# Performance work log

Hardware: AMD Instinct MI355X
Metric: run time of the kernel (lower is better)

Reference implementation:

```python
import jax, jax.numpy as jnp
from jax import lax
import numpy as np

C = 56; DI = 112; DS = 16; R = 4; K = 4; NB = 10; UP = 3
B, H, W = 1, 64, 64

def conv2d(x, w, b=None, pad=1, groups=1):
    out = lax.conv_general_dilated(x, w, (1, 1), [(pad, pad), (pad, pad)],
                                   feature_group_count=groups,
                                   dimension_numbers=('NCHW', 'OIHW', 'NCHW'))
    if b is not None:
        out = out + b[None, :, None, None]
    return out

def ln_last(x, w, b, eps=1e-5):
    mu = x.mean(-1, keepdims=True)
    var = ((x - mu) ** 2).mean(-1, keepdims=True)
    return (x - mu) / jnp.sqrt(var + eps) * w + b

def ln_cf(x, w, b, eps=1e-6):
    mu = x.mean(1, keepdims=True)
    var = ((x - mu) ** 2).mean(1, keepdims=True)
    return (x - mu) / jnp.sqrt(var + eps) * w[None, :, None, None] + b[None, :, None, None]

def bsconv(x, pw_w, dw_w, dw_b):
    x = conv2d(x, pw_w, pad=0)
    return conv2d(x, dw_w, dw_b, pad=1, groups=dw_w.shape[0])

def ss2d(x, p):
    # x: (B,H,W,C) -> SS2D (VMamba 4-direction selective scan)
    b, h, w, _ = x.shape
    L = h * w
    xz = x @ p['inproj_w'].T                        # (B,H,W,2*DI)
    xin, z = jnp.split(xz, 2, axis=-1)
    xc = jnp.transpose(xin, (0, 3, 1, 2))           # (B,DI,H,W)
    xc = jax.nn.silu(conv2d(xc, p['conv_w'], p['conv_b'], pad=1, groups=DI))
    xf = xc.reshape(b, DI, L)
    xt = jnp.swapaxes(xc, 2, 3).reshape(b, DI, L)
    x_hwwh = jnp.stack([xf, xt], axis=1)            # (B,2,DI,L)
    xs = jnp.concatenate([x_hwwh, jnp.flip(x_hwwh, -1)], axis=1)  # (B,K,DI,L)
    x_dbl = jnp.einsum('bkdl,kcd->bkcl', xs, p['xproj_w'])
    dts, Bs, Cs = jnp.split(x_dbl, [R, R + DS], axis=2)
    dts = jnp.einsum('bkrl,kdr->bkdl', dts, p['dt_w'])
    A = -jnp.exp(p['Alog'].reshape(K, DI, DS))
    delta = jax.nn.softplus(dts + p['dt_b'][None, :, :, None])    # (B,K,DI,L)

    def step(hst, inp):
        dl, xl, bl, cl = inp
        dA = jnp.exp(dl[..., None] * A[None])       # (B,K,DI,DS)
        hst = dA * hst + (dl * xl)[..., None] * bl[:, :, None, :]
        y = jnp.einsum('bkdn,bkn->bkd', hst, cl)
        return hst, y

    seq = (jnp.transpose(delta, (3, 0, 1, 2)), jnp.transpose(xs, (3, 0, 1, 2)),
           jnp.transpose(Bs, (3, 0, 1, 2)), jnp.transpose(Cs, (3, 0, 1, 2)))
    h0 = jnp.zeros((b, K, DI, DS), x.dtype)
    _, ys = lax.scan(step, h0, seq)                 # (L,B,K,DI)
    out_y = jnp.transpose(ys, (1, 2, 3, 0)) + p['D'].reshape(K, DI)[None, :, :, None] * xs
    inv = jnp.flip(out_y[:, 2:4], -1)
    y1 = out_y[:, 0]
    y2 = inv[:, 0]
    y3 = jnp.swapaxes(inv[:, 1].reshape(b, DI, w, h), 2, 3).reshape(b, DI, L)
    y4 = jnp.swapaxes(out_y[:, 1].reshape(b, DI, w, h), 2, 3).reshape(b, DI, L)
    y = jnp.swapaxes(y1 + y2 + y3 + y4, 1, 2).reshape(b, h, w, DI)
    y = ln_last(y, p['onorm_w'], p['onorm_b'])
    y = y * jax.nn.silu(z)
    return y @ p['outproj_w'].T

def safm(x, mfr_w, mfr_b, aggr_w, aggr_b):
    b, c, h, w = x.shape
    ch = c // 4
    parts = jnp.split(x, 4, axis=1)
    outs = []
    for i in range(4):
        s = parts[i]
        f = 2 ** i
        if i > 0:
            s = s.reshape(b, ch, h // f, f, w // f, f).max(axis=(3, 5))
        s = conv2d(s, mfr_w[i], mfr_b[i], pad=1, groups=ch)
        if i > 0:
            s = jnp.repeat(jnp.repeat(s, f, axis=2), f, axis=3)
        outs.append(s)
    out = conv2d(jnp.concatenate(outs, axis=1), aggr_w, aggr_b, pad=0)
    return jax.nn.gelu(out, approximate=False) * x

def afd(x, p):
    xn = jnp.transpose(x, (0, 2, 3, 1))
    xn = xn + ss2d(ln_last(xn, p['ln1_w'], p['ln1_b']), p)   # VSSBlock residual
    x = jnp.transpose(xn, (0, 3, 1, 2))
    x = x + safm(ln_cf(x, p['norm_w'], p['norm_b']), p['mfr_w'], p['mfr_b'], p['aggr_w'], p['aggr_b'])
    return x, x

def _forward(x, fea_pw_w, fea_dw_w, fea_dw_b,
             blk_ln1_w, blk_ln1_b, blk_inproj_w, blk_conv_w, blk_conv_b,
             blk_xproj_w, blk_dt_w, blk_dt_b, blk_Alog, blk_D,
             blk_onorm_w, blk_onorm_b, blk_outproj_w,
             blk_norm_w, blk_norm_b, blk_mfr_w, blk_mfr_b, blk_aggr_w, blk_aggr_b,
             c1_w, c1_b, norm_w, norm_b, c2_pw_w, c2_dw_w, c2_dw_b, up_w, up_b):
    out_fea = bsconv(x, fea_pw_w, fea_dw_w, fea_dw_b)
    bp = {'ln1_w': blk_ln1_w, 'ln1_b': blk_ln1_b, 'inproj_w': blk_inproj_w,
          'conv_w': blk_conv_w, 'conv_b': blk_conv_b, 'xproj_w': blk_xproj_w,
          'dt_w': blk_dt_w, 'dt_b': blk_dt_b, 'Alog': blk_Alog, 'D': blk_D,
          'onorm_w': blk_onorm_w, 'onorm_b': blk_onorm_b, 'outproj_w': blk_outproj_w,
          'norm_w': blk_norm_w, 'norm_b': blk_norm_b, 'mfr_w': blk_mfr_w,
          'mfr_b': blk_mfr_b, 'aggr_w': blk_aggr_w, 'aggr_b': blk_aggr_b}
    _, outs = lax.scan(afd, out_fea, bp)            # (NB,B,C,H,W) in B1..B10 order
    b, _, h, w = out_fea.shape
    trunk = jnp.transpose(outs, (1, 0, 2, 3, 4)).reshape(b, NB * C, h, w)
    out_B = conv2d(trunk, c1_w, c1_b, pad=0)
    out_B = jax.nn.gelu(ln_cf(out_B, norm_w, norm_b), approximate=False)
    out_lr = bsconv(out_B, c2_pw_w, c2_dw_w, c2_dw_b) + out_fea
    up = conv2d(out_lr, up_w, up_b, pad=1)          # (B, 3*UP*UP, H, W)
    oc = up.shape[1] // (UP * UP)
    ps = up.reshape(b, oc, UP, UP, h, w)
    return jnp.transpose(ps, (0, 1, 4, 2, 5, 3)).reshape(b, oc, h * UP, w * UP)

def setup_inputs():
    key = jax.random.key(0)
    ks = iter(jax.random.split(key, 40))
    rn = lambda shape, s=0.05: jax.random.normal(next(ks), shape, jnp.float32) * s
    ones = lambda shape: jnp.ones(shape, jnp.float32)
    zeros = lambda shape: jnp.zeros(shape, jnp.float32)
    return {
        'x': jax.random.normal(next(ks), (B, 3, H, W), jnp.float32),
        'fea_pw_w': rn((C, 3, 1, 1), 0.3),
        'fea_dw_w': rn((C, 1, 3, 3), 0.3),
        'fea_dw_b': zeros((C,)),
        'blk_ln1_w': ones((NB, C)), 'blk_ln1_b': zeros((NB, C)),
        'blk_inproj_w': rn((NB, 2 * DI, C)),
        'blk_conv_w': rn((NB, DI, 1, 3, 3), 0.2), 'blk_conv_b': zeros((NB, DI)),
        'blk_xproj_w': rn((NB, K, R + 2 * DS, DI)),
        'blk_dt_w': rn((NB, K, DI, R), 0.2),
        'blk_dt_b': jnp.full((NB, K, DI), -4.6, jnp.float32),
        'blk_Alog': jnp.broadcast_to(jnp.log(jnp.arange(1, DS + 1, dtype=jnp.float32)), (NB, K * DI, DS)) + jnp.zeros((NB, K * DI, DS), jnp.float32),
        'blk_D': ones((NB, K * DI)),
        'blk_onorm_w': ones((NB, DI)), 'blk_onorm_b': zeros((NB, DI)),
        'blk_outproj_w': rn((NB, C, DI)),
        'blk_norm_w': ones((NB, C)), 'blk_norm_b': zeros((NB, C)),
        'blk_mfr_w': rn((NB, 4, C // 4, 1, 3, 3), 0.2), 'blk_mfr_b': zeros((NB, 4, C // 4)),
        'blk_aggr_w': rn((NB, C, C, 1, 1)), 'blk_aggr_b': zeros((NB, C)),
        'c1_w': rn((C, NB * C, 1, 1)), 'c1_b': zeros((C,)),
        'norm_w': ones((C,)), 'norm_b': zeros((C,)),
        'c2_pw_w': rn((C, C, 1, 1)), 'c2_dw_w': rn((C, 1, 3, 3), 0.2), 'c2_dw_b': zeros((C,)),
        'up_w': rn((3 * UP * UP, C, 3, 3)), 'up_b': zeros((3 * UP * UP,)),
    }

def reference(x, fea_pw_w, fea_dw_w, fea_dw_b,
              blk_ln1_w, blk_ln1_b, blk_inproj_w, blk_conv_w, blk_conv_b,
              blk_xproj_w, blk_dt_w, blk_dt_b, blk_Alog, blk_D,
              blk_onorm_w, blk_onorm_b, blk_outproj_w,
              blk_norm_w, blk_norm_b, blk_mfr_w, blk_mfr_b, blk_aggr_w, blk_aggr_b,
              c1_w, c1_b, norm_w, norm_b, c2_pw_w, c2_dw_w, c2_dw_b, up_w, up_b):
    return _forward(x, fea_pw_w, fea_dw_w, fea_dw_b,
                    blk_ln1_w, blk_ln1_b, blk_inproj_w, blk_conv_w, blk_conv_b,
                    blk_xproj_w, blk_dt_w, blk_dt_b, blk_Alog, blk_D,
                    blk_onorm_w, blk_onorm_b, blk_outproj_w,
                    blk_norm_w, blk_norm_b, blk_mfr_w, blk_mfr_b, blk_aggr_w, blk_aggr_b,
                    c1_w, c1_b, norm_w, norm_b, c2_pw_w, c2_dw_w, c2_dw_b, up_w, up_b)
```

## Files before the change

### kernel.cpp

```cpp
#include <hip/hip_runtime.h>
#include <hip/hip_bf16.h>

#define HW 64
#define L4 4096
#define CC 56
#define DI 112
#define DSN 16
#define NBLK 10

typedef const float* BP;

__device__ __forceinline__ float bf(BP p, int i) { return p[i]; }
__device__ __forceinline__ float siluf(float x) { return x / (1.f + __expf(-x)); }
__device__ __forceinline__ float geluf(float x) { return 0.5f * x * (1.f + erff(x * 0.70710678f)); }

__global__ void k_fea_pw(BP x, BP w, float* __restrict__ t0) {
    int tid = blockIdx.x * blockDim.x + threadIdx.x;
    if (tid >= CC * L4) return;
    int c = tid >> 12, l = tid & 4095;
    float acc = 0.f;
    for (int i = 0; i < 3; ++i) acc += bf(x, i * L4 + l) * bf(w, c * 3 + i);
    t0[tid] = acc;
}

__global__ void __launch_bounds__(256) k_dw3x3t(
        const float* __restrict__ src, BP w, BP bvec, float* __restrict__ dst,
        int act, const float* __restrict__ addsrc) {
    int c = blockIdx.x >> 4;
    int tile = blockIdx.x & 15;
    int y0 = (tile >> 2) * 16, x0 = (tile & 3) * 16;
    __shared__ float sT[18 * 18];
    const float* sc = src + (size_t)c * L4;
    for (int idx = threadIdx.x; idx < 324; idx += 256) {
        int iy = idx / 18, ix = idx - iy * 18;
        int gy = y0 - 1 + iy, gx = x0 - 1 + ix;
        sT[idx] = (gy >= 0 && gy < 64 && gx >= 0 && gx < 64) ? sc[gy * 64 + gx] : 0.f;
    }
    __syncthreads();
    int py = threadIdx.x >> 4, px = threadIdx.x & 15;
    BP wr = w + c * 9;
    float acc = bvec ? bvec[c] : 0.f;
    #pragma unroll
    for (int ky = 0; ky < 3; ++ky)
        #pragma unroll
        for (int kx = 0; kx < 3; ++kx)
            acc += sT[(py + ky) * 18 + px + kx] * wr[ky * 3 + kx];
    if (act) acc = siluf(acc);
    int l = (y0 + py) * 64 + x0 + px;
    if (addsrc) acc += addsrc[(size_t)c * L4 + l];
    dst[(size_t)c * L4 + l] = acc;
}

__global__ void __launch_bounds__(256) k_ln56g(
        const float* __restrict__ part, BP bias, BP w, BP b, float* __restrict__ dst) {
    int lane = threadIdx.x & 63;
    int cg = threadIdx.x >> 6;
    int l0 = blockIdx.x * 64;
    __shared__ float sS[56 * 64];
    __shared__ float sPa[4][64], sPb[4][64];
    __shared__ float sMu[64], sRs[64];
    float ps = 0.f, ps2 = 0.f;
    for (int c = cg * 14; c < cg * 14 + 14; ++c) {
        float v = bias[c];
        #pragma unroll
        for (int z = 0; z < 5; ++z)
            v += part[(size_t)(z * 56 + c) * L4 + l0 + lane];
        sS[c * 64 + lane] = v; ps += v; ps2 += v * v;
    }
    sPa[cg][lane] = ps; sPb[cg][lane] = ps2;
    __syncthreads();
    if (threadIdx.x < 64) {
        float s = sPa[0][lane] + sPa[1][lane] + sPa[2][lane] + sPa[3][lane];
        float s2 = sPb[0][lane] + sPb[1][lane] + sPb[2][lane] + sPb[3][lane];
        float mu = s / 56.f;
        float var = fmaxf(s2 / 56.f - mu * mu, 0.f);
        sMu[lane] = mu; sRs[lane] = rsqrtf(var + 1e-6f);
    }
    __syncthreads();
    float mu = sMu[lane], rs = sRs[lane];
    for (int c = cg * 14; c < cg * 14 + 14; ++c) {
        float v = (sS[c * 64 + lane] - mu) * rs * w[c] + b[c];
        dst[(size_t)c * L4 + l0 + lane] = geluf(v);
    }
}

__global__ void __launch_bounds__(256) k_gemm(
        const float* __restrict__ src, BP w, BP bvec, const float* __restrict__ addsrc,
        float* __restrict__ dst, int nin, int nout) {
    int lane = threadIdx.x & 63;
    int jg = threadIdx.x >> 6;
    int l0 = blockIdx.x * 64;
    int j0 = blockIdx.y * 16;
    __shared__ __align__(16) float sS[56 * 64];
    __shared__ __align__(16) float sw[16 * 56];
    float acc[4] = {0.f, 0.f, 0.f, 0.f};

    for (int i0 = 0; i0 < nin; i0 += 56) {
        __syncthreads();
        for (int idx = threadIdx.x; idx < 56 * 64; idx += 256) {
            int ii = idx >> 6, px = idx & 63;
            sS[idx] = src[(size_t)(i0 + ii) * L4 + l0 + px];
        }
        for (int idx = threadIdx.x; idx < 16 * 56; idx += 256) {
            int jj = idx / 56, ii = idx - jj * 56;
            int j = j0 + jj;
            sw[idx] = (j < nout) ? w[(size_t)j * nin + i0 + ii] : 0.f;
        }
        __syncthreads();
        #pragma unroll
        for (int ii = 0; ii < 56; ii += 4) {
            float s0 = sS[(ii + 0) * 64 + lane];
            float s1 = sS[(ii + 1) * 64 + lane];
            float s2 = sS[(ii + 2) * 64 + lane];
            float s3 = sS[(ii + 3) * 64 + lane];
            #pragma unroll
            for (int jj = 0; jj < 4; ++jj) {
                const float4 wv = *(const float4*)&sw[(jg * 4 + jj) * 56 + ii];
                acc[jj] += s0 * wv.x + s1 * wv.y + s2 * wv.z + s3 * wv.w;
            }
        }
    }
    int l = l0 + lane;
    #pragma unroll
    for (int jj = 0; jj < 4; ++jj) {
        int j = j0 + jg * 4 + jj;
        if (j >= nout) continue;
        float v = acc[jj];
        if (bvec) v += bf(bvec, j);
        size_t idx = (size_t)j * L4 + l;
        if (addsrc) v += addsrc[idx];
        dst[idx] = v;
    }
}

__global__ void __launch_bounds__(256) k_c1(
        const float* __restrict__ src, BP w, float* __restrict__ part) {
    int lane = threadIdx.x & 63;
    int jg = threadIdx.x >> 6;
    int l0 = blockIdx.x * 64;
    int j0 = blockIdx.y * 16;
    int z = blockIdx.z;
    __shared__ __align__(16) float sS[56 * 64];
    __shared__ __align__(16) float sw[16 * 56];
    float acc[4] = {0.f, 0.f, 0.f, 0.f};

    for (int i0 = z * 112; i0 < z * 112 + 112; i0 += 56) {
        __syncthreads();
        for (int idx = threadIdx.x; idx < 56 * 64; idx += 256) {
            int ii = idx >> 6, px = idx & 63;
            sS[idx] = src[(size_t)(i0 + ii) * L4 + l0 + px];
        }
        for (int idx = threadIdx.x; idx < 16 * 56; idx += 256) {
            int jj = idx / 56, ii = idx - jj * 56;
            int j = j0 + jj;
            sw[idx] = (j < 56) ? w[(size_t)j * 560 + i0 + ii] : 0.f;
        }
        __syncthreads();
        #pragma unroll
        for (int ii = 0; ii < 56; ii += 4) {
            float s0 = sS[(ii + 0) * 64 + lane];
            float s1 = sS[(ii + 1) * 64 + lane];
            float s2 = sS[(ii + 2) * 64 + lane];
            float s3 = sS[(ii + 3) * 64 + lane];
            #pragma unroll
            for (int jj = 0; jj < 4; ++jj) {
                const float4 wv = *(const float4*)&sw[(jg * 4 + jj) * 56 + ii];
                acc[jj] += s0 * wv.x + s1 * wv.y + s2 * wv.z + s3 * wv.w;
            }
        }
    }
    int l = l0 + lane;
    #pragma unroll
    for (int jj = 0; jj < 4; ++jj) {
        int j = j0 + jg * 4 + jj;
        if (j < 56) part[(size_t)(z * 56 + j) * L4 + l] = acc[jj];
    }
}

__global__ void __launch_bounds__(256) k_xproj(
        const float* __restrict__ src, BP w, float* __restrict__ dst) {
    int lane = threadIdx.x & 31;
    int jg = threadIdx.x >> 5;
    int l0 = blockIdx.x * 32;
    int j0 = blockIdx.y * 16;
    __shared__ __align__(16) float sS[112 * 32];
    __shared__ __align__(16) float sw[16 * 112];
    float acc[2] = {0.f, 0.f};

    for (int idx = threadIdx.x; idx < 112 * 32; idx += 256) {
        int ii = idx >> 5, px = idx & 31;
        sS[idx] = src[(size_t)ii * L4 + l0 + px];
    }
    for (int idx = threadIdx.x; idx < 16 * 112; idx += 256) {
        int jj = idx / 112, ii = idx - jj * 112;
        sw[idx] = w[(size_t)(j0 + jj) * 112 + ii];
    }
    __syncthreads();
    #pragma unroll
    for (int ii = 0; ii < 112; ii += 4) {
        float s0 = sS[(ii + 0) * 32 + lane];
        float s1 = sS[(ii + 1) * 32 + lane];
        float s2 = sS[(ii + 2) * 32 + lane];
        float s3 = sS[(ii + 3) * 32 + lane];
        #pragma unroll
        for (int jj = 0; jj < 2; ++jj) {
            const float4 wv = *(const float4*)&sw[(jg * 2 + jj) * 112 + ii];
            acc[jj] += s0 * wv.x + s1 * wv.y + s2 * wv.z + s3 * wv.w;
        }
    }
    __syncthreads();
    #pragma unroll
    for (int jj = 0; jj < 2; ++jj)
        sS[(jg * 2 + jj) * 32 + lane] = acc[jj];
    __syncthreads();
    for (int idx = threadIdx.x; idx < 16 * 32; idx += 256) {
        int cidx = idx & 15, l2 = idx >> 4;
        int j = j0 + cidx;
        int k = j / 36, c = j - k * 36;
        dst[((size_t)k * L4 + l0 + l2) * 36 + c] = sS[cidx * 32 + l2];
    }
}

__global__ void __launch_bounds__(256) k_gemm_ln(
        const float* __restrict__ src, BP lnw, BP lnb, BP w,
        float* __restrict__ dst, int nout) {
    int lane = threadIdx.x & 63;
    int jg = threadIdx.x >> 6;
    int l0 = blockIdx.x * 64;
    int j0 = blockIdx.y * 16;
    __shared__ __align__(16) float sS[56 * 64];
    __shared__ __align__(16) float sw[16 * 56];
    __shared__ float sLw[56], sLb[56];
    float acc[4] = {0.f, 0.f, 0.f, 0.f};

    for (int idx = threadIdx.x; idx < 56 * 64; idx += 256) {
        int ii = idx >> 6, px = idx & 63;
        sS[idx] = src[(size_t)ii * L4 + l0 + px];
    }
    for (int idx = threadIdx.x; idx < 16 * 56; idx += 256) {
        int jj = idx / 56, ii = idx - jj * 56;
        int j = j0 + jj;
        sw[idx] = (j < nout) ? w[(size_t)j * 56 + ii] : 0.f;
    }
    if (threadIdx.x < 56) { sLw[threadIdx.x] = lnw[threadIdx.x]; sLb[threadIdx.x] = lnb[threadIdx.x]; }
    __syncthreads();
    if (threadIdx.x < 64) {
        int px = threadIdx.x;
        float s = 0.f, s2 = 0.f;
        for (int ii = 0; ii < 56; ++ii) { float v = sS[ii * 64 + px]; s += v; s2 += v * v; }
        float mu = s / 56.f;
        float var = fmaxf(s2 / 56.f - mu * mu, 0.f);
        float rstd = rsqrtf(var + 1e-5f);
        for (int ii = 0; ii < 56; ++ii)
            sS[ii * 64 + px] = (sS[ii * 64 + px] - mu) * rstd * sLw[ii] + sLb[ii];
    }
    __syncthreads();
    #pragma unroll
    for (int ii = 0; ii < 56; ii += 4) {
        float s0 = sS[(ii + 0) * 64 + lane];
        float s1 = sS[(ii + 1) * 64 + lane];
        float s2 = sS[(ii + 2) * 64 + lane];
        float s3 = sS[(ii + 3) * 64 + lane];
        #pragma unroll
        for (int jj = 0; jj < 4; ++jj) {
            const float4 wv = *(const float4*)&sw[(jg * 4 + jj) * 56 + ii];
            acc[jj] += s0 * wv.x + s1 * wv.y + s2 * wv.z + s3 * wv.w;
        }
    }
    int l = l0 + lane;
    #pragma unroll
    for (int jj = 0; jj < 4; ++jj) {
        int j = j0 + jg * 4 + jj;
        if (j < nout) dst[(size_t)j * L4 + l] = acc[jj];
    }
}

#define SPAD(p) ((p) + ((p) >> 5))
__global__ void __launch_bounds__(1024) k_scan(
        const float* __restrict__ xc, const float* __restrict__ pk,
        BP Alog, BP dtw, BP dtb, float* __restrict__ ybuf) {
    int pair = blockIdx.x;
    int n = threadIdx.x & 15;
    int c = threadIdx.x >> 4;
    int k = pair / DI, d = pair - k * DI;
    float a = -__expf(Alog[pair * DSN + n]);
    float w0 = dtw[pair * 4 + 0], w1 = dtw[pair * 4 + 1];
    float w2 = dtw[pair * 4 + 2], w3 = dtw[pair * 4 + 3];
    float db = dtb[pair];
    const float* xptr = xc + (size_t)d * L4;
    const float* pkk = pk + (size_t)k * L4 * 36;
    float* yptr = ybuf + (size_t)pair * L4;

    __shared__ float sDl[4224];
    __shared__ float sDlx[4224];
    __shared__ float sP[64 * 16];
    __shared__ float sHe[64 * 16];

    for (int p = threadIdx.x; p < L4; p += 1024) {
        const float* row = pkk + (size_t)p * 36;
        float v = db + row[0] * w0 + row[1] * w1 + row[2] * w2 + row[3] * w3;
        float dl = fmaxf(v, 0.f) + __logf(1.f + __expf(-fabsf(v)));
        sDl[SPAD(p)] = dl;
        sDlx[SPAD(p)] = dl * xptr[p];
    }
    __syncthreads();

    int p0, dp;
    if (k == 0)      { p0 = c * 64;        dp = 1;   }
    else if (k == 1) { p0 = c;             dp = 64;  }
    else if (k == 2) { p0 = 4095 - c * 64; dp = -1;  }
    else             { p0 = 4095 - c;      dp = -64; }
    long rstep = (long)dp * 36;

    float h = 0.f, P = 1.f;
    {
        int p = p0;
        const float* rB = pkk + (size_t)p0 * 36 + 4 + n;
        #pragma unroll 4
        for (int j = 0; j < 64; ++j) {
            int q = SPAD(p);
            float e = __expf(sDl[q] * a);
            h = e * h + sDlx[q] * (*rB);
            P *= e;
            p += dp; rB += rstep;
        }
    }
    int idx = c * 16 + n;
    sP[idx] = P;
    sHe[idx] = h;
    __syncthreads();

    for (int off = 1; off < 64; off <<= 1) {
        float pC = sP[idx], hC = sHe[idx];
        float pL = 0.f, hL = 0.f;
        if (c >= off) { pL = sP[idx - off * 16]; hL = sHe[idx - off * 16]; }
        __syncthreads();
        if (c >= off) { sP[idx] = pC * pL; sHe[idx] = pC * hL + hC; }
        __syncthreads();
    }

    h = (c > 0) ? sHe[idx - 16] : 0.f;
    {
        int p = p0;
        const float* rB = pkk + (size_t)p0 * 36 + 4 + n;
        const float* rC = pkk + (size_t)p0 * 36 + 20 + n;
        #pragma unroll 4
        for (int j = 0; j < 64; ++j) {
            int q = SPAD(p);
            float e = __expf(sDl[q] * a);
            h = e * h + sDlx[q] * (*rB);
            float y = h * (*rC);
            y += __shfl_xor(y, 1, 16);
            y += __shfl_xor(y, 2, 16);
            y += __shfl_xor(y, 4, 16);
            y += __shfl_xor(y, 8, 16);
            if (n == 0) yptr[p] = y;
            p += dp; rB += rstep; rC += rstep;
        }
    }
}

__global__ void __launch_bounds__(256) k_comb_proj(
        const float* __restrict__ ybuf, const float* __restrict__ xc,
        const float* __restrict__ zbuf, BP Dp, BP ow, BP ob, BP opw,
        const float* __restrict__ xin, BP nw, BP nbv,
        float* __restrict__ x_mid, float* __restrict__ xln) {
    int lane = threadIdx.x & 15;
    int grp = threadIdx.x >> 4;
    int l0 = blockIdx.x * 16;
    __shared__ __align__(16) float sY[112 * 16];
    __shared__ __align__(16) float sW[56 * 112];
    __shared__ float sPa[16][16], sPb[16][16];
    __shared__ float sMu[16], sRs[16];

    float ps = 0.f, ps2 = 0.f;
    for (int d = grp * 7; d < grp * 7 + 7; ++d) {
        float Ds = Dp[d] + Dp[DI + d] + Dp[2 * DI + d] + Dp[3 * DI + d];
        float v = ybuf[(size_t)d * L4 + l0 + lane]
                + ybuf[(size_t)(DI + d) * L4 + l0 + lane]
                + ybuf[(size_t)(2 * DI + d) * L4 + l0 + lane]
                + ybuf[(size_t)(3 * DI + d) * L4 + l0 + lane]
                + Ds * xc[(size_t)d * L4 + l0 + lane];
        sY[d * 16 + lane] = v; ps += v; ps2 += v * v;
    }
    sPa[grp][lane] = ps; sPb[grp][lane] = ps2;
    for (int idx = threadIdx.x; idx < 56 * 112; idx += 256) sW[idx] = opw[idx];
    __syncthreads();
    if (threadIdx.x < 16) {
        float s = 0.f, s2 = 0.f;
        for (int g = 0; g < 16; ++g) { s += sPa[g][lane]; s2 += sPb[g][lane]; }
        float mu = s / 112.f;
        float var = fmaxf(s2 / 112.f - mu * mu, 0.f);
        sMu[lane] = mu; sRs[lane] = rsqrtf(var + 1e-5f);
    }
    __syncthreads();
    {
        float mu = sMu[lane], rs = sRs[lane];
        for (int d = grp * 7; d < grp * 7 + 7; ++d) {
            float v = (sY[d * 16 + lane] - mu) * rs * ow[d] + ob[d];
            float z = zbuf[(size_t)d * L4 + l0 + lane];
            sY[d * 16 + lane] = v * siluf(z);
        }
    }
    __syncthreads();

    float acc[4] = {0.f, 0.f, 0.f, 0.f};
    #pragma unroll 2
    for (int ii = 0; ii < 112; ii += 4) {
        float s0 = sY[(ii + 0) * 16 + lane];
        float s1 = sY[(ii + 1) * 16 + lane];
        float s2 = sY[(ii + 2) * 16 + lane];
        float s3 = sY[(ii + 3) * 16 + lane];
        #pragma unroll
        for (int jj = 0; jj < 4; ++jj) {
            int j = grp * 4 + jj;
            if (j < 56) {
                const float4 wv = *(const float4*)&sW[j * 112 + ii];
                acc[jj] += s0 * wv.x + s1 * wv.y + s2 * wv.z + s3 * wv.w;
            }
        }
    }
    int l = l0 + lane;
    float vout[4];
    float ps3 = 0.f, ps4 = 0.f;
    #pragma unroll
    for (int jj = 0; jj < 4; ++jj) {
        int j = grp * 4 + jj;
        vout[jj] = 0.f;
        if (j < 56) {
            float v = acc[jj] + xin[(size_t)j * L4 + l];
            vout[jj] = v;
            x_mid[(size_t)j * L4 + l] = v;
            ps3 += v; ps4 += v * v;
        }
    }
    __syncthreads();
    sPa[grp][lane] = ps3; sPb[grp][lane] = ps4;
    __syncthreads();
    if (threadIdx.x < 16) {
        float s = 0.f, s2 = 0.f;
        for (int g = 0; g < 16; ++g) { s += sPa[g][lane]; s2 += sPb[g][lane]; }
        float mu = s / 56.f;
        float var = fmaxf(s2 / 56.f - mu * mu, 0.f);
        sMu[lane] = mu; sRs[lane] = rsqrtf(var + 1e-6f);
    }
    __syncthreads();
    {
        float mu = sMu[lane], rs = sRs[lane];
        #pragma unroll
        for (int jj = 0; jj < 4; ++jj) {
            int j = grp * 4 + jj;
            if (j < 56) xln[(size_t)j * L4 + l] = (vout[jj] - mu) * rs * nw[j] + nbv[j];
        }
    }
}

__global__ void __launch_bounds__(256) k_safm(
        const float* __restrict__ xln, BP mw, BP mb,
        float* __restrict__ s0, float* __restrict__ s1,
        float* __restrict__ s2, float* __restrict__ s3) {
    int b = blockIdx.x;
    if (b < 224) {
        int c = b >> 4;
        int tile = b & 15;
        int y0 = (tile >> 2) * 16, x0 = (tile & 3) * 16;
        __shared__ float sT[18 * 18];
        const float* sc = xln + (size_t)c * L4;
        for (int idx = threadIdx.x; idx < 324; idx += 256) {
            int iy = idx / 18, ix = idx - iy * 18;
            int gy = y0 - 1 + iy, gx = x0 - 1 + ix;
            sT[idx] = (gy >= 0 && gy < 64 && gx >= 0 && gx < 64) ? sc[gy * 64 + gx] : 0.f;
        }
        __syncthreads();
        int py = threadIdx.x >> 4, px = threadIdx.x & 15;
        BP wr = mw + c * 9;
        float acc = mb[c];
        #pragma unroll
        for (int ky = 0; ky < 3; ++ky)
            #pragma unroll
            for (int kx = 0; kx < 3; ++kx)
                acc += sT[(py + ky) * 18 + px + kx] * wr[ky * 3 + kx];
        s0[c * L4 + (y0 + py) * 64 + x0 + px] = acc;
    } else {
        int bb = b - 224;
        int i = bb / 14 + 1;
        int c = bb % 14;
        int S = 64 >> i;
        int f = 1 << i;
        __shared__ float sP[34 * 34];
        int W2 = S + 2;
        for (int idx = threadIdx.x; idx < W2 * W2; idx += 256) sP[idx] = 0.f;
        __syncthreads();
        const float* sc = xln + (size_t)(i * 14 + c) * L4;
        for (int cell = threadIdx.x; cell < S * S; cell += 256) {
            int y = cell / S, x = cell - y * S;
            float m = -3.4e38f;
            for (int dy = 0; dy < f; ++dy)
                for (int dx = 0; dx < f; ++dx)
                    m = fmaxf(m, sc[(y * f + dy) * 64 + x * f + dx]);
            sP[(y + 1) * W2 + x + 1] = m;
        }
        __syncthreads();
        BP wr = mw + (i * 14 + c) * 9;
        float bias = mb[i * 14 + c];
        float* dst = (i == 1) ? s1 : (i == 2) ? s2 : s3;
        for (int cell = threadIdx.x; cell < S * S; cell += 256) {
            int y = cell / S, x = cell - y * S;
            float acc = bias;
            #pragma unroll
            for (int ky = 0; ky < 3; ++ky)
                #pragma unroll
                for (int kx = 0; kx < 3; ++kx)
                    acc += sP[(y + ky) * W2 + x + kx] * wr[ky * 3 + kx];
            dst[c * S * S + cell] = acc;
        }
    }
}

__global__ void k_aggr(const float* __restrict__ s0, const float* __restrict__ s1,
                       const float* __restrict__ s2, const float* __restrict__ s3,
                       const float* __restrict__ xln, const float* __restrict__ x_mid,
                       BP aw, BP ab, float* __restrict__ out) {
    int tid = blockIdx.x * blockDim.x + threadIdx.x;
    if (tid >= CC * L4) return;
    int c = tid >> 12, l = tid & 4095;
    int h = l >> 6, w = l & 63;
    int o1 = (h >> 1) * 32 + (w >> 1);
    int o2 = (h >> 2) * 16 + (w >> 2);
    int o3 = (h >> 3) * 8 + (w >> 3);
    float acc = bf(ab, c);
    BP wr = aw + c * 56;
    for (int cg = 0; cg < 14; ++cg) acc += s0[cg * 4096 + l]  * bf(wr, cg);
    for (int cg = 0; cg < 14; ++cg) acc += s1[cg * 1024 + o1] * bf(wr, 14 + cg);
    for (int cg = 0; cg < 14; ++cg) acc += s2[cg * 256 + o2]  * bf(wr, 28 + cg);
    for (int cg = 0; cg < 14; ++cg) acc += s3[cg * 64 + o3]   * bf(wr, 42 + cg);
    out[tid] = x_mid[tid] + geluf(acc) * xln[tid];
}

__global__ void __launch_bounds__(256) k_up(
        const float* __restrict__ out_lr, BP uw, BP ub, float* __restrict__ out) {
    __shared__ float sIn[56 * 36];
    __shared__ float sW[27 * 56 * 9];
    int b = blockIdx.x;
    int y0 = (b >> 4) * 4, x0 = (b & 15) * 4;
    for (int idx = threadIdx.x; idx < 56 * 36; idx += 256) {
        int cc = idx / 36; int rem = idx - cc * 36; int iy = rem / 6, ix = rem - iy * 6;
        int gy = y0 - 1 + iy, gx = x0 - 1 + ix;
        sIn[idx] = (gy >= 0 && gy < 64 && gx >= 0 && gx < 64)
                 ? out_lr[(size_t)cc * L4 + gy * 64 + gx] : 0.f;
    }
    for (int idx = threadIdx.x; idx < 27 * 56 * 9; idx += 256) sW[idx] = uw[idx];
    __syncthreads();
    int px = threadIdx.x & 15;
    int og = threadIdx.x >> 4;
    int dy = px >> 2, dx = px & 3;
    for (int oo = 0; oo < 2; ++oo) {
        int o = og * 2 + oo;
        if (o >= 27) break;
        float acc = ub[o];
        const float* wb = &sW[o * 504];
        for (int cc = 0; cc < 56; ++cc) {
            const float* ib = &sIn[cc * 36 + dy * 6 + dx];
            const float* wc = wb + cc * 9;
            acc += ib[0] * wc[0] + ib[1] * wc[1] + ib[2] * wc[2]
                 + ib[6] * wc[3] + ib[7] * wc[4] + ib[8] * wc[5]
                 + ib[12] * wc[6] + ib[13] * wc[7] + ib[14] * wc[8];
        }
        int h = y0 + dy, wv = x0 + dx;
        int ch = o / 9, rr = (o % 9) / 3, ss = o % 3;
        out[ch * 36864 + (h * 3 + rr) * 192 + (wv * 3 + ss)] = acc;
    }
}

extern "C" void kernel_launch(void* const* d_in, const int* in_sizes, int n_in,
                              void* d_out, int out_size, void* d_ws, size_t ws_size,
                              hipStream_t stream) {
    BP in0  = (BP)d_in[0];
    BP in1  = (BP)d_in[1];
    BP in2  = (BP)d_in[2];
    BP in3  = (BP)d_in[3];
    BP in4  = (BP)d_in[4];
    BP in5  = (BP)d_in[5];
    BP in6  = (BP)d_in[6];
    BP in7  = (BP)d_in[7];
    BP in8  = (BP)d_in[8];
    BP in9  = (BP)d_in[9];
    BP in10 = (BP)d_in[10];
    BP in11 = (BP)d_in[11];
    BP in12 = (BP)d_in[12];
    BP in13 = (BP)d_in[13];
    BP in14 = (BP)d_in[14];
    BP in15 = (BP)d_in[15];
    BP in16 = (BP)d_in[16];
    BP in17 = (BP)d_in[17];
    BP in18 = (BP)d_in[18];
    BP in19 = (BP)d_in[19];
    BP in20 = (BP)d_in[20];
    BP in21 = (BP)d_in[21];
    BP in22 = (BP)d_in[22];
    BP in23 = (BP)d_in[23];
    BP in24 = (BP)d_in[24];
    BP in25 = (BP)d_in[25];
    BP in26 = (BP)d_in[26];
    BP in27 = (BP)d_in[27];
    BP in28 = (BP)d_in[28];
    BP in29 = (BP)d_in[29];
    BP in30 = (BP)d_in[30];
    BP in31 = (BP)d_in[31];

    float* ws = (float*)d_ws;
    float* trunk   = ws; ws += 560 * L4;
    float* out_fea = ws; ws += CC * L4;
    float* t0      = ws; ws += CC * L4;
    float* xz      = ws; ws += 224 * L4;
    float* xc      = ws; ws += DI * L4;
    float* pk      = ws; ws += 4 * 36 * L4;
    float* ybuf    = ws; ws += 4 * DI * L4;
    float* x_mid   = ws; ws += CC * L4;
    float* xln     = ws; ws += CC * L4;
    float* s0      = ws; ws += 14 * 4096;
    float* s1      = ws; ws += 14 * 1024;
    float* s2      = ws; ws += 14 * 256;
    float* s3      = ws; ws += 14 * 64;
    float* part    = ws; ws += 5 * 56 * L4;
    float* gB      = ws; ws += CC * L4;
    float* tbuf    = ws; ws += CC * L4;
    float* out_lr  = ws; ws += CC * L4;

    auto nb256 = [](int n) { return dim3((n + 255) / 256); };
    auto gemm_grid = [](int nout) { return dim3(64, (nout + 15) / 16); };

    k_fea_pw<<<nb256(CC * L4), 256, 0, stream>>>(in0, in1, t0);
    k_dw3x3t<<<dim3(CC * 16), 256, 0, stream>>>(t0, in2, in3, out_fea, 0, nullptr);

    for (int nb = 0; nb < NBLK; ++nb) {
        const float* xin = (nb == 0) ? out_fea : trunk + (size_t)(nb - 1) * CC * L4;
        float* xout = trunk + (size_t)nb * CC * L4;
        BP ln1w = in4 + nb * 56,        ln1b = in5 + nb * 56;
        BP ipw  = in6 + nb * 224 * 56;
        BP cw   = in7 + nb * 112 * 9,   cb   = in8 + nb * 112;
        BP xpw  = in9 + nb * 4 * 36 * 112;
        BP dtw  = in10 + nb * 4 * 112 * 4, dtb = in11 + nb * 448;
        BP alog = in12 + nb * 448 * 16, Dp   = in13 + nb * 448;
        BP onw  = in14 + nb * 112,      onb  = in15 + nb * 112;
        BP opw  = in16 + nb * 56 * 112;
        BP nw   = in17 + nb * 56,       nbv  = in18 + nb * 56;
        BP mw   = in19 + nb * 4 * 14 * 9, mb = in20 + nb * 56;
        BP aw   = in21 + nb * 56 * 56,  ab   = in22 + nb * 56;

        k_gemm_ln<<<gemm_grid(224), 256, 0, stream>>>(xin, ln1w, ln1b, ipw, xz, 224);
        k_dw3x3t<<<dim3(DI * 16), 256, 0, stream>>>(xz, cw, cb, xc, 1, nullptr);
        k_xproj<<<dim3(128, 9), 256, 0, stream>>>(xc, xpw, pk);
        k_scan<<<dim3(4 * DI), 1024, 0, stream>>>(xc, pk, alog, dtw, dtb, ybuf);
        k_comb_proj<<<dim3(256), 256, 0, stream>>>(ybuf, xc, xz + 112 * L4, Dp, onw, onb, opw,
                                                   xin, nw, nbv, x_mid, xln);
        k_safm<<<dim3(266), 256, 0, stream>>>(xln, mw, mb, s0, s1, s2, s3);
        k_aggr<<<nb256(CC * L4), 256, 0, stream>>>(s0, s1, s2, s3, xln, x_mid, aw, ab, xout);
    }

    k_c1<<<dim3(64, 4, 5), 256, 0, stream>>>(trunk, in23, part);
    k_ln56g<<<dim3(64), 256, 0, stream>>>(part, in24, in25, in26, gB);
    k_gemm<<<gemm_grid(56), 256, 0, stream>>>(gB, in27, nullptr, nullptr, tbuf, 56, 56);
    k_dw3x3t<<<dim3(CC * 16), 256, 0, stream>>>(tbuf, in28, in29, out_lr, 0, out_fea);
    k_up<<<dim3(256), 256, 0, stream>>>(out_lr, in30, in31, (float*)d_out);
}
```

Baseline: 1.300 ms.

## Batch scan loads and stage scan outputs in shared memory for coalesced writes

The selective-scan kernel now loads B, C and the decay terms for four steps before running the recurrence, so memory latency overlaps with the dependent chain. Per-step outputs go into a padded shared buffer, and the whole block then writes them to global memory in linear order instead of scattered single-lane stores. It also uses a float4 load for the dt projection inputs and adds a launch-bounds occupancy hint. The cost is about 16KB more shared memory per block and one extra barrier.

New measurement: 1.297 ms. No clear change (-0.2%).

```diff
diff --git a/kernel.cpp b/kernel.cpp
--- a/kernel.cpp
+++ b/kernel.cpp
@@ -276,7 +276,7 @@
 }
 
 #define SPAD(p) ((p) + ((p) >> 5))
-__global__ void __launch_bounds__(1024) k_scan(
+__global__ void __launch_bounds__(1024, 8) k_scan(
         const float* __restrict__ xc, const float* __restrict__ pk,
         BP Alog, BP dtw, BP dtb, float* __restrict__ ybuf) {
     int pair = blockIdx.x;
@@ -295,10 +295,11 @@
     __shared__ float sDlx[4224];
     __shared__ float sP[64 * 16];
     __shared__ float sHe[64 * 16];
+    __shared__ float sY[64 * 65];
 
     for (int p = threadIdx.x; p < L4; p += 1024) {
-        const float* row = pkk + (size_t)p * 36;
-        float v = db + row[0] * w0 + row[1] * w1 + row[2] * w2 + row[3] * w3;
+        const float4 r4 = *(const float4*)(pkk + (size_t)p * 36);
+        float v = db + r4.x * w0 + r4.y * w1 + r4.z * w2 + r4.w * w3;
         float dl = fmaxf(v, 0.f) + __logf(1.f + __expf(-fabsf(v)));
         sDl[SPAD(p)] = dl;
         sDlx[SPAD(p)] = dl * xptr[p];
@@ -316,13 +317,21 @@
     {
         int p = p0;
         const float* rB = pkk + (size_t)p0 * 36 + 4 + n;
-        #pragma unroll 4
-        for (int j = 0; j < 64; ++j) {
-            int q = SPAD(p);
-            float e = __expf(sDl[q] * a);
-            h = e * h + sDlx[q] * (*rB);
-            P *= e;
-            p += dp; rB += rstep;
+        for (int jb = 0; jb < 64; jb += 4) {
+            float Bv[4], ev[4], dxv[4];
+            #pragma unroll
+            for (int u = 0; u < 4; ++u) {
+                int q = SPAD(p + u * dp);
+                Bv[u] = rB[u * rstep];
+                ev[u] = __expf(sDl[q] * a);
+                dxv[u] = sDlx[q];
+            }
+            #pragma unroll
+            for (int u = 0; u < 4; ++u) {
+                h = ev[u] * h + dxv[u] * Bv[u];
+                P *= ev[u];
+            }
+            p += 4 * dp; rB += 4 * rstep;
         }
     }
     int idx = c * 16 + n;
@@ -344,19 +353,37 @@
         int p = p0;
         const float* rB = pkk + (size_t)p0 * 36 + 4 + n;
         const float* rC = pkk + (size_t)p0 * 36 + 20 + n;
-        #pragma unroll 4
-        for (int j = 0; j < 64; ++j) {
-            int q = SPAD(p);
-            float e = __expf(sDl[q] * a);
-            h = e * h + sDlx[q] * (*rB);
-            float y = h * (*rC);
-            y += __shfl_xor(y, 1, 16);
-            y += __shfl_xor(y, 2, 16);
-            y += __shfl_xor(y, 4, 16);
-            y += __shfl_xor(y, 8, 16);
-            if (n == 0) yptr[p] = y;
-            p += dp; rB += rstep; rC += rstep;
-        }
+        for (int jb = 0; jb < 64; jb += 4) {
+            float Bv[4], Cv[4], ev[4], dxv[4];
+            #pragma unroll
+            for (int u = 0; u < 4; ++u) {
+                int q = SPAD(p + u * dp);
+                Bv[u] = rB[u * rstep];
+                Cv[u] = rC[u * rstep];
+                ev[u] = __expf(sDl[q] * a);
+                dxv[u] = sDlx[q];
+            }
+            #pragma unroll
+            for (int u = 0; u < 4; ++u) {
+                h = ev[u] * h + dxv[u] * Bv[u];
+                float y = h * Cv[u];
+                y += __shfl_xor(y, 1, 16);
+                y += __shfl_xor(y, 2, 16);
+                y += __shfl_xor(y, 4, 16);
+                y += __shfl_xor(y, 8, 16);
+                if (n == 0) sY[c * 65 + jb + u] = y;
+            }
+            p += 4 * dp; rB += 4 * rstep; rC += 4 * rstep;
+        }
+    }
+    __syncthreads();
+
+    for (int pp = threadIdx.x; pp < L4; pp += 1024) {
+        int q = (k >= 2) ? (4095 - pp) : pp;
+        int cc, jj;
+        if (k & 1) { cc = q & 63; jj = q >> 6; }
+        else       { cc = q >> 6; jj = q & 63; }
+        yptr[pp] = sY[cc * 65 + jj];
     }
 }
 
```
